# Optimization experiments

Hardware: AMD Instinct MI355X
Metric: run time of the kernel (lower is better)

The kernel has to match this reference:

```python
import jax, jax.numpy as jnp
import numpy as np

B, F, O = 4096, 16384, 256
MANTISSA_BITS = 23  # flip only mantissa bits to keep values finite


def setup_inputs() -> dict:
    key = jax.random.key(0)
    k1, k2, k3, k4 = jax.random.split(key, 4)
    x = jax.random.normal(k1, (B, F), dtype=jnp.float32)
    W = jax.random.normal(k2, (F, O), dtype=jnp.float32) * 0.02
    b = jnp.zeros((O,), dtype=jnp.float32)
    bitswap_coeff = jnp.ones((), dtype=jnp.float32)  # scalar 'bitswap_coeff' weight
    # uniform categorical over flattened features == uniform randint
    idx = jax.random.randint(k3, (B,), 0, F, dtype=jnp.int32)
    bit_positions = jax.random.randint(k4, (B,), 0, MANTISSA_BITS, dtype=jnp.int32)
    return {"x": x, "W": W, "b": b, "bitswap_coeff": bitswap_coeff,
            "idx": idx, "bit_positions": bit_positions}


def _bit_flip(g, bit_positions):
    # SimulateSwap: flip one mantissa bit of the float32 representation
    gi = jax.lax.bitcast_convert_type(g, jnp.int32)
    gi = gi ^ (jnp.int32(1) << bit_positions)
    return jax.lax.bitcast_convert_type(gi, jnp.float32)


def reference(x, W, b, bitswap_coeff, idx, bit_positions):
    rows = jnp.arange(x.shape[0])
    # gather_nd(batch_dims=1): one element per batch row
    g = x[rows, idx]                              # [B]
    updates = _bit_flip(g, bit_positions) - g     # swap_sim(x) - x
    # tensor_scatter_nd_update onto zeros, scaled by bitswap coefficient
    pert = jnp.zeros_like(x).at[rows, idx].set(updates) * bitswap_coeff
    # wrapped layer: Dense
    return (x + pert) @ W + b
```

## Files before the change

### kernel.cpp

```cpp
#include <hip/hip_runtime.h>

#define M_DIM 4096
#define K_DIM 16384
#define N_DIM 256
#define SPLIT 8
#define BK 64
#define KSLICE (K_DIM / SPLIT)
#define NITER (KSLICE / BK)

typedef __bf16 bf16x8 __attribute__((ext_vector_type(8)));
typedef __bf16 bf16x4 __attribute__((ext_vector_type(4)));
typedef float f32x4 __attribute__((ext_vector_type(4)));

__global__ __launch_bounds__(256) void wt_kernel(const float* __restrict__ W,
                                                 __bf16* __restrict__ Wt) {
  __shared__ float tile[64][65];
  const int k0 = blockIdx.x * 64, n0 = blockIdx.y * 64;
  const int t = threadIdx.x;
#pragma unroll
  for (int r = 0; r < 4; ++r) {
    int idx4 = r * 256 + t;
    int kr = idx4 >> 4, c4 = idx4 & 15;
    f32x4 v = *(const f32x4*)(W + (size_t)(k0 + kr) * N_DIM + n0 + c4 * 4);
#pragma unroll
    for (int j = 0; j < 4; ++j) tile[kr][c4 * 4 + j] = v[j];
  }
  __syncthreads();
#pragma unroll
  for (int r = 0; r < 4; ++r) {
    int nr = (t >> 4) + r * 16, k4 = t & 15;
    bf16x4 o;
#pragma unroll
    for (int j = 0; j < 4; ++j) o[j] = (__bf16)tile[k4 * 4 + j][nr];
    *(bf16x4*)(Wt + (size_t)(n0 + nr) * K_DIM + k0 + k4 * 4) = o;
  }
}

__global__ __launch_bounds__(256, 3) void gemm_kernel(const float* __restrict__ x,
                                                      const __bf16* __restrict__ Wt,
                                                      __bf16* __restrict__ part) {
  __shared__ __bf16 As[64 * 72];
  __shared__ __bf16 Bs[256 * 72];

  const int t = threadIdx.x;
  const int l = t & 63;
  const int w = t >> 6;
  const int la = l & 15, q = l >> 4;
  const int m0 = blockIdx.x * 64;
  const int kbase = blockIdx.y * KSLICE;

  const int arow = t >> 4, ac4 = t & 15;
  const int bn = t >> 3, bk8 = (t & 7) * 8;

  const float* ap = x + (size_t)(m0 + arow) * K_DIM + kbase + ac4 * 4;
  const __bf16* bp = Wt + (size_t)bn * K_DIM + kbase + bk8;

  f32x4 areg[4];
  bf16x8 breg[8];

#pragma unroll
  for (int r = 0; r < 4; ++r) areg[r] = *(const f32x4*)(ap + (size_t)r * 16 * K_DIM);
#pragma unroll
  for (int c = 0; c < 8; ++c) breg[c] = *(const bf16x8*)(bp + (size_t)c * 32 * K_DIM);

  f32x4 acc[4][4];
  const f32x4 zero = {0.f, 0.f, 0.f, 0.f};
#pragma unroll
  for (int i = 0; i < 4; ++i)
#pragma unroll
    for (int j = 0; j < 4; ++j) acc[i][j] = zero;

  for (int it = 0; it < NITER; ++it) {
    __syncthreads();
#pragma unroll
    for (int r = 0; r < 4; ++r) {
      bf16x4 o = {(__bf16)areg[r][0], (__bf16)areg[r][1],
                  (__bf16)areg[r][2], (__bf16)areg[r][3]};
      *(bf16x4*)(&As[(arow + r * 16) * 72 + ac4 * 4]) = o;
    }
#pragma unroll
    for (int c = 0; c < 8; ++c)
      *(bf16x8*)(&Bs[(bn + c * 32) * 72 + bk8]) = breg[c];
    __syncthreads();

    if (it + 1 < NITER) {
      ap += BK;
      bp += BK;
#pragma unroll
      for (int r = 0; r < 4; ++r) areg[r] = *(const f32x4*)(ap + (size_t)r * 16 * K_DIM);
#pragma unroll
      for (int c = 0; c < 8; ++c) breg[c] = *(const bf16x8*)(bp + (size_t)c * 32 * K_DIM);
    }

#pragma unroll
    for (int ks = 0; ks < 2; ++ks) {
      const int kb = ks * 32 + q * 8;
      bf16x8 a[4], b[4];
#pragma unroll
      for (int i = 0; i < 4; ++i)
        a[i] = *(const bf16x8*)(&As[(i * 16 + la) * 72 + kb]);
#pragma unroll
      for (int j = 0; j < 4; ++j)
        b[j] = *(const bf16x8*)(&Bs[(w * 64 + j * 16 + la) * 72 + kb]);
#pragma unroll
      for (int i = 0; i < 4; ++i)
#pragma unroll
        for (int j = 0; j < 4; ++j)
          acc[i][j] = __builtin_amdgcn_mfma_f32_16x16x32_bf16(a[i], b[j], acc[i][j], 0, 0, 0);
    }
  }

  __bf16* pbase = part + (size_t)blockIdx.y * ((size_t)M_DIM * N_DIM);
#pragma unroll
  for (int i = 0; i < 4; ++i) {
    int r0 = m0 + i * 16 + q * 4;
#pragma unroll
    for (int j = 0; j < 4; ++j) {
      int c = w * 64 + j * 16 + la;
#pragma unroll
      for (int r = 0; r < 4; ++r)
        pbase[(size_t)(r0 + r) * N_DIM + c] = (__bf16)acc[i][j][r];
    }
  }
}

__global__ __launch_bounds__(256) void reduce_kernel(const __bf16* __restrict__ part,
                                                     const float* __restrict__ x,
                                                     const float* __restrict__ W,
                                                     const float* __restrict__ bvec,
                                                     const float* __restrict__ coeffp,
                                                     const int* __restrict__ idx,
                                                     const int* __restrict__ bp,
                                                     float* __restrict__ out) {
  const int row = blockIdx.x;
  const int o = threadIdx.x;
  const int iv = idx[row];
  const float g = x[(size_t)row * K_DIM + iv];
  const int bits = __float_as_int(g) ^ (1 << bp[row]);
  const float upd = __int_as_float(bits) - g;
  const float coeff = coeffp[0];
  const size_t off = (size_t)row * N_DIM + o;
  float sum = 0.f;
#pragma unroll
  for (int s = 0; s < SPLIT; ++s)
    sum += (float)part[(size_t)s * ((size_t)M_DIM * N_DIM) + off];
  out[off] = sum + coeff * upd * W[(size_t)iv * N_DIM + o] + bvec[o];
}

extern "C" void kernel_launch(void* const* d_in, const int* in_sizes, int n_in,
                              void* d_out, int out_size, void* d_ws, size_t ws_size,
                              hipStream_t stream) {
  const float* x = (const float*)d_in[0];
  const float* W = (const float*)d_in[1];
  const float* b = (const float*)d_in[2];
  const float* coeff = (const float*)d_in[3];
  const int* idx = (const int*)d_in[4];
  const int* bp = (const int*)d_in[5];
  float* out = (float*)d_out;

  __bf16* Wt = (__bf16*)d_ws;
  const size_t wt_bytes = (size_t)K_DIM * N_DIM * 2;
  __bf16* part = (__bf16*)((char*)d_ws + wt_bytes);

  hipLaunchKernelGGL(wt_kernel, dim3(K_DIM / 64, N_DIM / 64), dim3(256), 0, stream, W, Wt);
  hipLaunchKernelGGL(gemm_kernel, dim3(M_DIM / 64, SPLIT), dim3(256), 0, stream,
                     x, Wt, part);
  hipLaunchKernelGGL(reduce_kernel, dim3(M_DIM), dim3(256), 0, stream,
                     part, x, W, b, coeff, idx, bp, out);
}
```

Measured before the change: 413.5 us.

## Pre-tile W into swizzled K-blocks and stream via direct global-to-LDS double buffering

The transpose kernel now writes W as contiguous 64-wide K tiles with an XOR swizzle on the K offset. The GEMM loads each B tile straight into a double-buffered LDS region with global_load_lds, and A loads are prefetched two iterations ahead. This removes the register staging and LDS write path for B and overlaps the next tile's load with compute, with hand-placed waitcnt and barrier calls. In exchange LDS per block grows and the launch bound drops to 2 blocks per CU, which lowers occupancy.

```diff
diff --git a/kernel.cpp b/kernel.cpp
--- a/kernel.cpp
+++ b/kernel.cpp
@@ -1,4 +1,5 @@
 #include <hip/hip_runtime.h>
+#include <cstdint>
 
 #define M_DIM 4096
 #define K_DIM 16384
@@ -7,13 +8,14 @@
 #define BK 64
 #define KSLICE (K_DIM / SPLIT)
 #define NITER (KSLICE / BK)
+#define BTILE 16384
 
 typedef __bf16 bf16x8 __attribute__((ext_vector_type(8)));
 typedef __bf16 bf16x4 __attribute__((ext_vector_type(4)));
 typedef float f32x4 __attribute__((ext_vector_type(4)));
 
 __global__ __launch_bounds__(256) void wt_kernel(const float* __restrict__ W,
-                                                 __bf16* __restrict__ Wt) {
+                                                 __bf16* __restrict__ Wt2) {
   __shared__ float tile[64][65];
   const int k0 = blockIdx.x * 64, n0 = blockIdx.y * 64;
   const int t = threadIdx.x;
@@ -26,42 +28,53 @@
     for (int j = 0; j < 4; ++j) tile[kr][c4 * 4 + j] = v[j];
   }
   __syncthreads();
+  const size_t obase = (size_t)blockIdx.x * ((size_t)N_DIM * 64);
 #pragma unroll
   for (int r = 0; r < 4; ++r) {
     int nr = (t >> 4) + r * 16, k4 = t & 15;
+    int n = n0 + nr;
     bf16x4 o;
 #pragma unroll
     for (int j = 0; j < 4; ++j) o[j] = (__bf16)tile[k4 * 4 + j][nr];
-    *(bf16x4*)(Wt + (size_t)(n0 + nr) * K_DIM + k0 + k4 * 4) = o;
+    int kk = (k4 * 4) ^ ((n & 7) << 3);
+    *(bf16x4*)(Wt2 + obase + (size_t)n * 64 + kk) = o;
   }
 }
 
-__global__ __launch_bounds__(256, 3) void gemm_kernel(const float* __restrict__ x,
-                                                      const __bf16* __restrict__ Wt,
+__global__ __launch_bounds__(256, 2) void gemm_kernel(const float* __restrict__ x,
+                                                      const __bf16* __restrict__ Wt2,
                                                       __bf16* __restrict__ part) {
   __shared__ __bf16 As[64 * 72];
-  __shared__ __bf16 Bs[256 * 72];
+  __shared__ __bf16 Bs[2 * BTILE];
 
   const int t = threadIdx.x;
   const int l = t & 63;
   const int w = t >> 6;
   const int la = l & 15, q = l >> 4;
+  const int kx = (la & 7) << 3;
   const int m0 = blockIdx.x * 64;
-  const int kbase = blockIdx.y * KSLICE;
+  const int tile0 = blockIdx.y * (KSLICE / 64);
 
   const int arow = t >> 4, ac4 = t & 15;
-  const int bn = t >> 3, bk8 = (t & 7) * 8;
+  const float* ap = x + (size_t)(m0 + arow) * K_DIM + (size_t)blockIdx.y * KSLICE + ac4 * 4;
 
-  const float* ap = x + (size_t)(m0 + arow) * K_DIM + kbase + ac4 * 4;
-  const __bf16* bp = Wt + (size_t)bn * K_DIM + kbase + bk8;
+  const uint8_t* bgbase = (const uint8_t*)(Wt2 + (size_t)tile0 * BTILE);
 
-  f32x4 areg[4];
-  bf16x8 breg[8];
+  f32x4 aregA[4], aregB[4];
 
 #pragma unroll
-  for (int r = 0; r < 4; ++r) areg[r] = *(const f32x4*)(ap + (size_t)r * 16 * K_DIM);
+  for (int i = 0; i < 8; ++i) {
+    const int c = i * 4 + w;
+    __builtin_amdgcn_global_load_lds(
+        (const __attribute__((address_space(1))) void*)(bgbase + c * 1024 + l * 16),
+        (__attribute__((address_space(3))) void*)((uint8_t*)Bs + c * 1024),
+        16, 0, 0);
+  }
 #pragma unroll
-  for (int c = 0; c < 8; ++c) breg[c] = *(const bf16x8*)(bp + (size_t)c * 32 * K_DIM);
+  for (int r = 0; r < 4; ++r) aregA[r] = *(const f32x4*)(ap + (size_t)r * 16 * K_DIM);
+  ap += BK;
+#pragma unroll
+  for (int r = 0; r < 4; ++r) aregB[r] = *(const f32x4*)(ap + (size_t)r * 16 * K_DIM);
 
   f32x4 acc[4][4];
   const f32x4 zero = {0.f, 0.f, 0.f, 0.f};
@@ -70,45 +83,55 @@
 #pragma unroll
     for (int j = 0; j < 4; ++j) acc[i][j] = zero;
 
-  for (int it = 0; it < NITER; ++it) {
-    __syncthreads();
-#pragma unroll
-    for (int r = 0; r < 4; ++r) {
-      bf16x4 o = {(__bf16)areg[r][0], (__bf16)areg[r][1],
-                  (__bf16)areg[r][2], (__bf16)areg[r][3]};
-      *(bf16x4*)(&As[(arow + r * 16) * 72 + ac4 * 4]) = o;
-    }
-#pragma unroll
-    for (int c = 0; c < 8; ++c)
-      *(bf16x8*)(&Bs[(bn + c * 32) * 72 + bk8]) = breg[c];
-    __syncthreads();
+#define GEMM_ITER(IT, AREG, RBUF, WBUF)                                              \
+  {                                                                                  \
+    __builtin_amdgcn_s_barrier();         \
+    _Pragma("unroll") for (int r = 0; r < 4; ++r) {                                  \
+      bf16x4 o = {(__bf16)AREG[r][0], (__bf16)AREG[r][1],                            \
+                  (__bf16)AREG[r][2], (__bf16)AREG[r][3]};                           \
+      *(bf16x4*)(&As[(arow + r * 16) * 72 + ac4 * 4]) = o;                           \
+    }                                                                                \
+    if ((IT) + 1 < NITER)                                                            \
+      asm volatile("s_waitcnt vmcnt(4) lgkmcnt(0)" ::: "memory");                    \
+    else                                                                             \
+      asm volatile("s_waitcnt vmcnt(0) lgkmcnt(0)" ::: "memory");                    \
+    __builtin_amdgcn_s_barrier();             \
+    if ((IT) + 1 < NITER) {                                                          \
+      _Pragma("unroll") for (int i = 0; i < 8; ++i) {                                \
+        const int c = i * 4 + w;                                                     \
+        __builtin_amdgcn_global_load_lds(                                            \
+            (const __attribute__((address_space(1))) void*)(                         \
+                bgbase + ((IT) + 1) * 32768 + c * 1024 + l * 16),                    \
+            (__attribute__((address_space(3))) void*)(                               \
+                (uint8_t*)Bs + (WBUF)*32768 + c * 1024),                             \
+            16, 0, 0);                                                               \
+      }                                                                              \
+    }                                                                                \
+    if ((IT) + 2 < NITER) {                   \
+      ap += BK;                                                                      \
+      _Pragma("unroll") for (int r = 0; r < 4; ++r)                                  \
+          AREG[r] = *(const f32x4*)(ap + (size_t)r * 16 * K_DIM);                    \
+    }                                                                                \
+    const __bf16* bsb = Bs + (RBUF)*BTILE;                                           \
+    _Pragma("unroll") for (int ks = 0; ks < 2; ++ks) {                               \
+      const int kb = ks * 32 + q * 8;                                                \
+      bf16x8 a[4], b[4];                                                             \
+      _Pragma("unroll") for (int i = 0; i < 4; ++i)                                  \
+          a[i] = *(const bf16x8*)(&As[(i * 16 + la) * 72 + kb]);                     \
+      _Pragma("unroll") for (int j = 0; j < 4; ++j)                                  \
+          b[j] = *(const bf16x8*)(&bsb[(w * 64 + j * 16 + la) * 64 + (kb ^ kx)]);    \
+      _Pragma("unroll") for (int i = 0; i < 4; ++i)                                  \
+          _Pragma("unroll") for (int j = 0; j < 4; ++j)                              \
+              acc[i][j] =                                                            \
+          __builtin_amdgcn_mfma_f32_16x16x32_bf16(a[i], b[j], acc[i][j], 0, 0, 0);   \
+    }                                                                                \
+  }
 
-    if (it + 1 < NITER) {
-      ap += BK;
-      bp += BK;
-#pragma unroll
-      for (int r = 0; r < 4; ++r) areg[r] = *(const f32x4*)(ap + (size_t)r * 16 * K_DIM);
-#pragma unroll
-      for (int c = 0; c < 8; ++c) breg[c] = *(const bf16x8*)(bp + (size_t)c * 32 * K_DIM);
-    }
-
-#pragma unroll
-    for (int ks = 0; ks < 2; ++ks) {
-      const int kb = ks * 32 + q * 8;
-      bf16x8 a[4], b[4];
-#pragma unroll
-      for (int i = 0; i < 4; ++i)
-        a[i] = *(const bf16x8*)(&As[(i * 16 + la) * 72 + kb]);
-#pragma unroll
-      for (int j = 0; j < 4; ++j)
-        b[j] = *(const bf16x8*)(&Bs[(w * 64 + j * 16 + la) * 72 + kb]);
-#pragma unroll
-      for (int i = 0; i < 4; ++i)
-#pragma unroll
-        for (int j = 0; j < 4; ++j)
-          acc[i][j] = __builtin_amdgcn_mfma_f32_16x16x32_bf16(a[i], b[j], acc[i][j], 0, 0, 0);
-    }
+  for (int it = 0; it < NITER; it += 2) {
+    GEMM_ITER(it, aregA, 0, 1);
+    GEMM_ITER(it + 1, aregB, 1, 0);
   }
+#undef GEMM_ITER
 
   __bf16* pbase = part + (size_t)blockIdx.y * ((size_t)M_DIM * N_DIM);
 #pragma unroll
@@ -158,13 +181,13 @@
   const int* bp = (const int*)d_in[5];
   float* out = (float*)d_out;
 
-  __bf16* Wt = (__bf16*)d_ws;
+  __bf16* Wt2 = (__bf16*)d_ws;
   const size_t wt_bytes = (size_t)K_DIM * N_DIM * 2;
   __bf16* part = (__bf16*)((char*)d_ws + wt_bytes);
 
-  hipLaunchKernelGGL(wt_kernel, dim3(K_DIM / 64, N_DIM / 64), dim3(256), 0, stream, W, Wt);
+  hipLaunchKernelGGL(wt_kernel, dim3(K_DIM / 64, N_DIM / 64), dim3(256), 0, stream, W, Wt2);
   hipLaunchKernelGGL(gemm_kernel, dim3(M_DIM / 64, SPLIT), dim3(256), 0, stream,
-                     x, Wt, part);
+                     x, Wt2, part);
   hipLaunchKernelGGL(reduce_kernel, dim3(M_DIM), dim3(256), 0, stream,
                      part, x, W, b, coeff, idx, bp, out);
 }
```

Result: slower. 422.9 us (+2.3%).

## Pre-pack W into MFMA fragment layout and load operands directly to registers

Applied to the files above, without the earlier changes.

W is now pre-packed into a bf16 layout that matches the MFMA B-fragment order, so each lane reads its fragment straight from global memory. The GEMM no longer uses shared memory or barriers. A fragments are loaded from fp32 x straight into registers and converted there, with two k-step register buffers alternating for software prefetch. Each block becomes a 2x2 wave grid covering 32 rows by 128 columns per wave, and the grid is linearised so that split-K slices of the same row block sit next to each other. In exchange, register pressure rises (launch bounds drop to 2 blocks per SIMD), and each wave fetches its own copy of A and B with no shared-memory reuse across waves.

```diff
diff --git a/kernel.cpp b/kernel.cpp
--- a/kernel.cpp
+++ b/kernel.cpp
@@ -1,127 +1,119 @@
 #include <hip/hip_runtime.h>
+#include <cstdint>
 
 #define M_DIM 4096
 #define K_DIM 16384
 #define N_DIM 256
 #define SPLIT 8
-#define BK 64
 #define KSLICE (K_DIM / SPLIT)
-#define NITER (KSLICE / BK)
+#define NITER (KSLICE / 32)
 
 typedef __bf16 bf16x8 __attribute__((ext_vector_type(8)));
-typedef __bf16 bf16x4 __attribute__((ext_vector_type(4)));
 typedef float f32x4 __attribute__((ext_vector_type(4)));
 
 __global__ __launch_bounds__(256) void wt_kernel(const float* __restrict__ W,
-                                                 __bf16* __restrict__ Wt) {
-  __shared__ float tile[64][65];
-  const int k0 = blockIdx.x * 64, n0 = blockIdx.y * 64;
+                                                 __bf16* __restrict__ Bp) {
+  __shared__ float tile[32][257];
+  const int kb = blockIdx.x;
   const int t = threadIdx.x;
 #pragma unroll
-  for (int r = 0; r < 4; ++r) {
+  for (int r = 0; r < 8; ++r) {
     int idx4 = r * 256 + t;
-    int kr = idx4 >> 4, c4 = idx4 & 15;
-    f32x4 v = *(const f32x4*)(W + (size_t)(k0 + kr) * N_DIM + n0 + c4 * 4);
+    int kr = idx4 >> 6, c4 = idx4 & 63;
+    f32x4 v = *(const f32x4*)(W + (size_t)(kb * 32 + kr) * N_DIM + c4 * 4);
 #pragma unroll
-    for (int j = 0; j < 4; ++j) tile[kr][c4 * 4 + j] = v[j];
+    for (int u = 0; u < 4; ++u) tile[kr][c4 * 4 + u] = v[u];
   }
   __syncthreads();
 #pragma unroll
-  for (int r = 0; r < 4; ++r) {
-    int nr = (t >> 4) + r * 16, k4 = t & 15;
-    bf16x4 o;
+  for (int rr = 0; rr < 4; ++rr) {
+    int g = rr * 256 + t;
+    int j = g >> 6, l = g & 63;
+    int q = l >> 4, la = l & 15;
+    bf16x8 o;
 #pragma unroll
-    for (int j = 0; j < 4; ++j) o[j] = (__bf16)tile[k4 * 4 + j][nr];
-    *(bf16x4*)(Wt + (size_t)(n0 + nr) * K_DIM + k0 + k4 * 4) = o;
+    for (int e = 0; e < 8; ++e) o[e] = (__bf16)tile[q * 8 + e][j * 16 + la];
+    *(bf16x8*)(Bp + ((size_t)kb * 16 + j) * 512 + l * 8) = o;
   }
 }
 
-__global__ __launch_bounds__(256, 3) void gemm_kernel(const float* __restrict__ x,
-                                                      const __bf16* __restrict__ Wt,
+__global__ __launch_bounds__(256, 2) void gemm_kernel(const float* __restrict__ x,
+                                                      const __bf16* __restrict__ Bp,
                                                       __bf16* __restrict__ part) {
-  __shared__ __bf16 As[64 * 72];
-  __shared__ __bf16 Bs[256 * 72];
-
   const int t = threadIdx.x;
   const int l = t & 63;
   const int w = t >> 6;
+  const int rg = w & 1;
+  const int nh = w >> 1;
   const int la = l & 15, q = l >> 4;
-  const int m0 = blockIdx.x * 64;
-  const int kbase = blockIdx.y * KSLICE;
+  const int bid = blockIdx.x;
+  const int ysplit = bid & 7;
+  const int m0 = (bid >> 3) * 64;
+  const int kbase = ysplit * KSLICE;
 
-  const int arow = t >> 4, ac4 = t & 15;
-  const int bn = t >> 3, bk8 = (t & 7) * 8;
+  const int r0 = m0 + rg * 32 + la;
+  const float* ap0 = x + (size_t)r0 * K_DIM + kbase + q * 8;
+  const float* ap1 = ap0 + (size_t)16 * K_DIM;
 
-  const float* ap = x + (size_t)(m0 + arow) * K_DIM + kbase + ac4 * 4;
-  const __bf16* bp = Wt + (size_t)bn * K_DIM + kbase + bk8;
+  const __bf16* bq = Bp + ((size_t)(kbase >> 5) * 16 + (size_t)nh * 8) * 512 + l * 8;
 
-  f32x4 areg[4];
-  bf16x8 breg[8];
+  f32x4 aE[4], aO[4];
+  bf16x8 bE[8], bO[8];
 
+  aE[0] = *(const f32x4*)(ap0);      aE[1] = *(const f32x4*)(ap0 + 4);
+  aE[2] = *(const f32x4*)(ap1);      aE[3] = *(const f32x4*)(ap1 + 4);
+  aO[0] = *(const f32x4*)(ap0 + 32); aO[1] = *(const f32x4*)(ap0 + 36);
+  aO[2] = *(const f32x4*)(ap1 + 32); aO[3] = *(const f32x4*)(ap1 + 36);
+  ap0 += 64; ap1 += 64;
 #pragma unroll
-  for (int r = 0; r < 4; ++r) areg[r] = *(const f32x4*)(ap + (size_t)r * 16 * K_DIM);
+  for (int jn = 0; jn < 8; ++jn) bE[jn] = *(const bf16x8*)(bq + jn * 512);
 #pragma unroll
-  for (int c = 0; c < 8; ++c) breg[c] = *(const bf16x8*)(bp + (size_t)c * 32 * K_DIM);
+  for (int jn = 0; jn < 8; ++jn) bO[jn] = *(const bf16x8*)(bq + 8192 + jn * 512);
+  bq += 16384;
 
-  f32x4 acc[4][4];
+  f32x4 acc[16];
   const f32x4 zero = {0.f, 0.f, 0.f, 0.f};
 #pragma unroll
-  for (int i = 0; i < 4; ++i)
-#pragma unroll
-    for (int j = 0; j < 4; ++j) acc[i][j] = zero;
+  for (int i = 0; i < 16; ++i) acc[i] = zero;
 
-  for (int it = 0; it < NITER; ++it) {
-    __syncthreads();
-#pragma unroll
-    for (int r = 0; r < 4; ++r) {
-      bf16x4 o = {(__bf16)areg[r][0], (__bf16)areg[r][1],
-                  (__bf16)areg[r][2], (__bf16)areg[r][3]};
-      *(bf16x4*)(&As[(arow + r * 16) * 72 + ac4 * 4]) = o;
-    }
-#pragma unroll
-    for (int c = 0; c < 8; ++c)
-      *(bf16x8*)(&Bs[(bn + c * 32) * 72 + bk8]) = breg[c];
-    __syncthreads();
-
-    if (it + 1 < NITER) {
-      ap += BK;
-      bp += BK;
-#pragma unroll
-      for (int r = 0; r < 4; ++r) areg[r] = *(const f32x4*)(ap + (size_t)r * 16 * K_DIM);
-#pragma unroll
-      for (int c = 0; c < 8; ++c) breg[c] = *(const bf16x8*)(bp + (size_t)c * 32 * K_DIM);
-    }
-
-#pragma unroll
-    for (int ks = 0; ks < 2; ++ks) {
-      const int kb = ks * 32 + q * 8;
-      bf16x8 a[4], b[4];
-#pragma unroll
-      for (int i = 0; i < 4; ++i)
-        a[i] = *(const bf16x8*)(&As[(i * 16 + la) * 72 + kb]);
-#pragma unroll
-      for (int j = 0; j < 4; ++j)
-        b[j] = *(const bf16x8*)(&Bs[(w * 64 + j * 16 + la) * 72 + kb]);
-#pragma unroll
-      for (int i = 0; i < 4; ++i)
-#pragma unroll
-        for (int j = 0; j < 4; ++j)
-          acc[i][j] = __builtin_amdgcn_mfma_f32_16x16x32_bf16(a[i], b[j], acc[i][j], 0, 0, 0);
-    }
+#define STEP(KS, AR, BR, AOFF, BOFF)                                                 \
+  {                                                                                  \
+    bf16x8 af0, af1;                                                                 \
+    _Pragma("unroll") for (int e = 0; e < 4; ++e) {                                  \
+      af0[e] = (__bf16)AR[0][e]; af0[e + 4] = (__bf16)AR[1][e];                      \
+      af1[e] = (__bf16)AR[2][e]; af1[e + 4] = (__bf16)AR[3][e];                      \
+    }                                                                                \
+    if ((KS) + 2 < NITER) {                     \
+      AR[0] = *(const f32x4*)(ap0 + (AOFF));      AR[1] = *(const f32x4*)(ap0 + (AOFF) + 4); \
+      AR[2] = *(const f32x4*)(ap1 + (AOFF));      AR[3] = *(const f32x4*)(ap1 + (AOFF) + 4); \
+    }                                                                                \
+    _Pragma("unroll") for (int jn = 0; jn < 8; ++jn) {                               \
+      acc[jn] = __builtin_amdgcn_mfma_f32_16x16x32_bf16(af0, BR[jn], acc[jn], 0, 0, 0); \
+      acc[8 + jn] =                                                                  \
+          __builtin_amdgcn_mfma_f32_16x16x32_bf16(af1, BR[jn], acc[8 + jn], 0, 0, 0); \
+      if ((KS) + 2 < NITER)    \
+        BR[jn] = *(const bf16x8*)(bq + (BOFF) + jn * 512);                           \
+    }                                                                                \
   }
 
-  __bf16* pbase = part + (size_t)blockIdx.y * ((size_t)M_DIM * N_DIM);
+  for (int ks = 0; ks < NITER; ks += 2) {
+    STEP(ks, aE, bE, 0, 0)
+    STEP(ks + 1, aO, bO, 32, 8192)
+    ap0 += 64; ap1 += 64; bq += 16384;
+  }
+#undef STEP
+
+  __bf16* pbase = part + (size_t)ysplit * ((size_t)M_DIM * N_DIM);
+  const int orow = m0 + rg * 32 + q * 4;
+  const int ocol = nh * 128 + la;
 #pragma unroll
-  for (int i = 0; i < 4; ++i) {
-    int r0 = m0 + i * 16 + q * 4;
+  for (int mt = 0; mt < 2; ++mt)
 #pragma unroll
-    for (int j = 0; j < 4; ++j) {
-      int c = w * 64 + j * 16 + la;
+    for (int jn = 0; jn < 8; ++jn)
 #pragma unroll
       for (int r = 0; r < 4; ++r)
-        pbase[(size_t)(r0 + r) * N_DIM + c] = (__bf16)acc[i][j][r];
-    }
-  }
+        pbase[(size_t)(orow + mt * 16 + r) * N_DIM + ocol + jn * 16] =
+            (__bf16)acc[mt * 8 + jn][r];
 }
 
 __global__ __launch_bounds__(256) void reduce_kernel(const __bf16* __restrict__ part,
@@ -158,13 +150,13 @@
   const int* bp = (const int*)d_in[5];
   float* out = (float*)d_out;
 
-  __bf16* Wt = (__bf16*)d_ws;
-  const size_t wt_bytes = (size_t)K_DIM * N_DIM * 2;
-  __bf16* part = (__bf16*)((char*)d_ws + wt_bytes);
+  __bf16* Bp = (__bf16*)d_ws;
+  const size_t bp_bytes = (size_t)K_DIM * N_DIM * 2;
+  __bf16* part = (__bf16*)((char*)d_ws + bp_bytes);
 
-  hipLaunchKernelGGL(wt_kernel, dim3(K_DIM / 64, N_DIM / 64), dim3(256), 0, stream, W, Wt);
-  hipLaunchKernelGGL(gemm_kernel, dim3(M_DIM / 64, SPLIT), dim3(256), 0, stream,
-                     x, Wt, part);
+  hipLaunchKernelGGL(wt_kernel, dim3(K_DIM / 32), dim3(256), 0, stream, W, Bp);
+  hipLaunchKernelGGL(gemm_kernel, dim3((M_DIM / 64) * SPLIT), dim3(256), 0, stream,
+                     x, Bp, part);
   hipLaunchKernelGGL(reduce_kernel, dim3(M_DIM), dim3(256), 0, stream,
                      part, x, W, b, coeff, idx, bp, out);
 }
```

Result: slower. 429.6 us (+3.9%).
